# Optimization experiments

Measured on AMD Instinct MI355X. Metric: run time of the kernel, lower is better.

## Reference

```python
import jax, jax.numpy as jnp
import numpy as np

N, E = 50000, 800000          # nodes, directed edges (before self-loops)
IN, H, C = 128, 8, 32         # in_feats, heads, per-head channels (= h_feats)
G = 64                        # graphs in batch
NEG_SLOPE = 0.2               # PyG GATConv default leaky_relu slope


def setup_inputs() -> dict:
    key = jax.random.key(0)
    ks = jax.random.split(key, 8)
    x = jax.random.normal(ks[0], (N, IN), jnp.float32)
    edge_index = jax.random.randint(ks[1], (2, E), 0, N)
    batch = jnp.sort(jax.random.randint(ks[2], (N,), 0, G))
    W = jax.random.normal(ks[3], (IN, H * C), jnp.float32) * 0.05
    att_src = jax.random.normal(ks[4], (H, C), jnp.float32) * 0.1
    att_dst = jax.random.normal(ks[5], (H, C), jnp.float32) * 0.1
    bias = jnp.zeros((C,), jnp.float32)
    lin_w = jax.random.normal(ks[6], (C, 2), jnp.float32) * 0.1
    lin_b = jnp.zeros((2,), jnp.float32)
    return dict(x=x, edge_index=edge_index, batch=batch, W=W,
                att_src=att_src, att_dst=att_dst, bias=bias,
                lin_w=lin_w, lin_b=lin_b)


def gat_conv(x, edge_index, W, att_src, att_dst, bias):
    # PyG GATConv, heads=H, concat=False, add_self_loops=True
    n = x.shape[0]
    h = (x @ W).reshape(n, H, C)                      # [N,H,C]
    loops = jnp.arange(n, dtype=edge_index.dtype)
    src = jnp.concatenate([edge_index[0], loops])     # [E+N]
    dst = jnp.concatenate([edge_index[1], loops])
    a_src = jnp.einsum('nhc,hc->nh', h, att_src)      # [N,H]
    a_dst = jnp.einsum('nhc,hc->nh', h, att_dst)
    e = jax.nn.leaky_relu(a_src[src] + a_dst[dst], NEG_SLOPE)  # [E+N,H]
    # segment softmax over edges sharing the same destination node
    m = jax.ops.segment_max(e, dst, num_segments=n)
    m = jnp.where(jnp.isfinite(m), m, 0.0)            # guard isolated nodes
    w = jnp.exp(e - m[dst])
    denom = jax.ops.segment_sum(w, dst, num_segments=n)
    alpha = w / (denom[dst] + 1e-16)                  # [E+N,H]
    out = jax.ops.segment_sum(h[src] * alpha[:, :, None], dst, num_segments=n)  # [N,H,C]
    return out.mean(axis=1) + bias                    # concat=False -> head mean


def reference(x, edge_index, batch, W, att_src, att_dst, bias, lin_w, lin_b):
    hid = jax.nn.relu(gat_conv(x, edge_index, W, att_src, att_dst, bias))  # [N,C]
    sums = jax.ops.segment_sum(hid, batch, num_segments=G)                  # [G,C]
    cnt = jax.ops.segment_sum(jnp.ones((hid.shape[0],), hid.dtype), batch,
                              num_segments=G)
    pooled = sums / jnp.maximum(cnt, 1.0)[:, None]    # global_mean_pool
    # Dropout(0.5) is identity in eval mode
    x_t = pooled @ lin_w + lin_b                      # [G,2]
    return (x_t, pooled)
```

## Files before the change

kernel.cpp:

```cpp
#include <hip/hip_runtime.h>
#include <hip/hip_bf16.h>

#define N_NODES 50000
#define E_EDGES 800000
#define IN_F 128
#define H_HEADS 8
#define C_CH 32
#define HC 256
#define G_GRAPHS 64
#define NEG_SLOPE 0.2f

__global__ __launch_bounds__(256) void k_gemm(const float* __restrict__ x,
        const float* __restrict__ W, const float* __restrict__ att_src,
        const float* __restrict__ att_dst, float* __restrict__ h,
        float* __restrict__ a_src, float* __restrict__ a_dst) {
    __shared__ float xs[8 * IN_F];
    const int n0 = blockIdx.x * 8;
    const int tid = threadIdx.x;
    ((float4*)xs)[tid] = ((const float4*)(x + (size_t)n0 * IN_F))[tid];
    __syncthreads();

    const int j = tid;
    float acc[8];
    #pragma unroll
    for (int r = 0; r < 8; ++r) acc[r] = 0.f;

    const float4* xs4 = (const float4*)xs;
    for (int k4 = 0; k4 < IN_F / 4; ++k4) {
        const float w0 = W[(k4 * 4 + 0) * HC + j];
        const float w1 = W[(k4 * 4 + 1) * HC + j];
        const float w2 = W[(k4 * 4 + 2) * HC + j];
        const float w3 = W[(k4 * 4 + 3) * HC + j];
        #pragma unroll
        for (int r = 0; r < 8; ++r) {
            float4 xv = xs4[r * (IN_F / 4) + k4];
            acc[r] += xv.x * w0 + xv.y * w1 + xv.z * w2 + xv.w * w3;
        }
    }

    const float asv = att_src[j], adv = att_dst[j];
    const int hh = j >> 5;
    #pragma unroll
    for (int r = 0; r < 8; ++r) {
        h[(size_t)(n0 + r) * HC + j] = acc[r];
        float s = acc[r] * asv, d = acc[r] * adv;
        #pragma unroll
        for (int off = 16; off; off >>= 1) {
            s += __shfl_xor(s, off, 64);
            d += __shfl_xor(d, off, 64);
        }
        if ((tid & 31) == 0) {
            a_src[(n0 + r) * H_HEADS + hh] = s;
            a_dst[(n0 + r) * H_HEADS + hh] = d;
        }
    }
}

__global__ __launch_bounds__(256) void k_hist(const int* __restrict__ ei,
        int* __restrict__ deg) {
    int i = blockIdx.x * 256 + threadIdx.x;
    if (i < E_EDGES) atomicAdd(deg + ei[E_EDGES + i], 1);
}

__global__ __launch_bounds__(1024) void k_scan(const int* __restrict__ deg,
        int* __restrict__ off, int* __restrict__ cursor) {
    __shared__ int carry;
    __shared__ int wsum[16];
    const int tid = threadIdx.x, lane = tid & 63, wid = tid >> 6;
    if (tid == 0) carry = 0;
    __syncthreads();
    for (int base = 0; base < N_NODES; base += 1024) {
        int i = base + tid;
        int v = (i < N_NODES) ? deg[i] : 0;
        int s = v;
        #pragma unroll
        for (int d = 1; d < 64; d <<= 1) {
            int t = __shfl_up(s, d, 64);
            if (lane >= d) s += t;
        }
        if (lane == 63) wsum[wid] = s;
        __syncthreads();
        if (wid == 0 && lane < 16) {
            int t = wsum[lane];
            #pragma unroll
            for (int d = 1; d < 16; d <<= 1) {
                int u = __shfl_up(t, d, 64);
                if (lane >= d) t += u;
            }
            wsum[lane] = t;
        }
        __syncthreads();
        int wpre = wid ? wsum[wid - 1] : 0;
        int excl = carry + wpre + s - v;
        if (i < N_NODES) { off[i] = excl; cursor[i] = excl; }
        __syncthreads();
        if (tid == 0) carry += wsum[15];
        __syncthreads();
    }
    if (tid == 0) off[N_NODES] = E_EDGES;
}

__global__ __launch_bounds__(256) void k_scatter(const int* __restrict__ ei,
        int* __restrict__ cursor, int* __restrict__ csr_src) {
    int i = blockIdx.x * 256 + threadIdx.x;
    if (i >= E_EDGES) return;
    int dst = ei[E_EDGES + i];
    int p = atomicAdd(cursor + dst, 1);
    csr_src[p] = ei[i];
}

__global__ __launch_bounds__(256) void k_node(const float* __restrict__ h,
        const float* __restrict__ a_src, const float* __restrict__ a_dst,
        const int* __restrict__ off, const int* __restrict__ csr_src,
        const int* __restrict__ batch, const float* __restrict__ bias,
        float* __restrict__ pool, float* __restrict__ cnt) {
    const int wave = threadIdx.x >> 6, lane = threadIdx.x & 63;
    const int n = blockIdx.x * 4 + wave;
    if (n >= N_NODES) return;
    const int hh = lane >> 3;
    const int beg = off[n], end = off[n + 1];
    const float adst = a_dst[n * H_HEADS + hh];
    float es = a_src[n * H_HEADS + hh] + adst;
    const float e_self = es > 0.f ? es : NEG_SLOPE * es;

    float m = e_self;
    for (int k = beg; k < end; ++k) {
        int src = csr_src[k];
        float e = a_src[src * H_HEADS + hh] + adst;
        e = e > 0.f ? e : NEG_SLOPE * e;
        m = fmaxf(m, e);
    }

    float denom = 0.f;
    float4 acc = {0.f, 0.f, 0.f, 0.f};
    {
        float w = __expf(e_self - m);
        denom += w;
        float4 hv = ((const float4*)(h + (size_t)n * HC))[lane];
        acc.x += w * hv.x; acc.y += w * hv.y;
        acc.z += w * hv.z; acc.w += w * hv.w;
    }
    int k = beg;
    for (; k + 1 < end; k += 2) {
        int s0 = csr_src[k], s1 = csr_src[k + 1];
        float e0 = a_src[s0 * H_HEADS + hh] + adst;
        float e1 = a_src[s1 * H_HEADS + hh] + adst;
        e0 = e0 > 0.f ? e0 : NEG_SLOPE * e0;
        e1 = e1 > 0.f ? e1 : NEG_SLOPE * e1;
        float w0 = __expf(e0 - m);
        float w1 = __expf(e1 - m);
        float4 h0 = ((const float4*)(h + (size_t)s0 * HC))[lane];
        float4 h1 = ((const float4*)(h + (size_t)s1 * HC))[lane];
        denom += w0 + w1;
        acc.x += w0 * h0.x + w1 * h1.x;
        acc.y += w0 * h0.y + w1 * h1.y;
        acc.z += w0 * h0.z + w1 * h1.z;
        acc.w += w0 * h0.w + w1 * h1.w;
    }
    if (k < end) {
        int s0 = csr_src[k];
        float e0 = a_src[s0 * H_HEADS + hh] + adst;
        e0 = e0 > 0.f ? e0 : NEG_SLOPE * e0;
        float w0 = __expf(e0 - m);
        float4 h0 = ((const float4*)(h + (size_t)s0 * HC))[lane];
        denom += w0;
        acc.x += w0 * h0.x; acc.y += w0 * h0.y;
        acc.z += w0 * h0.z; acc.w += w0 * h0.w;
    }

    const float inv = 1.f / (denom + 1e-16f);
    float4 r = {acc.x * inv, acc.y * inv, acc.z * inv, acc.w * inv};
    #pragma unroll
    for (int o = 8; o < 64; o <<= 1) {
        r.x += __shfl_xor(r.x, o, 64);
        r.y += __shfl_xor(r.y, o, 64);
        r.z += __shfl_xor(r.z, o, 64);
        r.w += __shfl_xor(r.w, o, 64);
    }
    if (lane < 8) {
        const int c0 = lane * 4;
        const int g = batch[n];
        float o0 = fmaxf(r.x * 0.125f + bias[c0 + 0], 0.f);
        float o1 = fmaxf(r.y * 0.125f + bias[c0 + 1], 0.f);
        float o2 = fmaxf(r.z * 0.125f + bias[c0 + 2], 0.f);
        float o3 = fmaxf(r.w * 0.125f + bias[c0 + 3], 0.f);
        float* pg = pool + g * C_CH + c0;
        atomicAdd(pg + 0, o0); atomicAdd(pg + 1, o1);
        atomicAdd(pg + 2, o2); atomicAdd(pg + 3, o3);
        if (lane == 0) atomicAdd(cnt + g, 1.f);
    }
}

__global__ __launch_bounds__(256) void k_final(const float* __restrict__ pool,
        const float* __restrict__ cnt, const float* __restrict__ lin_w,
        const float* __restrict__ lin_b, float* __restrict__ out) {
    __shared__ float pd[G_GRAPHS * C_CH];
    int t = threadIdx.x;
    for (int i = t; i < G_GRAPHS * C_CH; i += 256) {
        int g = i >> 5;
        float p = pool[i] / fmaxf(cnt[g], 1.f);
        pd[i] = p;
        out[G_GRAPHS * 2 + i] = p;
    }
    __syncthreads();
    if (t < G_GRAPHS * 2) {
        int g = t >> 1, o = t & 1;
        float s = lin_b[o];
        #pragma unroll
        for (int c = 0; c < C_CH; ++c) s += pd[g * C_CH + c] * lin_w[c * 2 + o];
        out[t] = s;
    }
}

extern "C" void kernel_launch(void* const* d_in, const int* in_sizes, int n_in,
                              void* d_out, int out_size, void* d_ws, size_t ws_size,
                              hipStream_t stream) {
    const float* x       = (const float*)d_in[0];
    const int*   ei      = (const int*)d_in[1];
    const int*   batch   = (const int*)d_in[2];
    const float* W       = (const float*)d_in[3];
    const float* att_src = (const float*)d_in[4];
    const float* att_dst = (const float*)d_in[5];
    const float* bias    = (const float*)d_in[6];
    const float* lin_w   = (const float*)d_in[7];
    const float* lin_b   = (const float*)d_in[8];

    char* ws = (char*)d_ws;
    float* h       = (float*)(ws);
    float* a_src   = (float*)(ws + 51200000);
    float* a_dst   = (float*)(ws + 52800000);
    int*   deg     = (int*)  (ws + 54400000);
    int*   off     = (int*)  (ws + 54600000);
    int*   cursor  = (int*)  (ws + 54800064);
    int*   csr_src = (int*)  (ws + 55000064);
    float* pool    = (float*)(ws + 58200064);
    float* cnt     = (float*)(ws + 58208256);

    hipMemsetAsync(deg, 0, 200000, stream);
    hipMemsetAsync(pool, 0, 8192 + 256, stream);

    k_gemm<<<N_NODES / 8, 256, 0, stream>>>(x, W, att_src, att_dst, h, a_src, a_dst);
    k_hist<<<(E_EDGES + 255) / 256, 256, 0, stream>>>(ei, deg);
    k_scan<<<1, 1024, 0, stream>>>(deg, off, cursor);
    k_scatter<<<(E_EDGES + 255) / 256, 256, 0, stream>>>(ei, cursor, csr_src);
    k_node<<<(N_NODES + 3) / 4, 256, 0, stream>>>(
        h, a_src, a_dst, off, csr_src, batch, bias, pool, cnt);
    k_final<<<1, 256, 0, stream>>>(pool, cnt, lin_w, lin_b, (float*)d_out);
}
```

Measured before the change: 817.7 us.

## Store projected features as bf16, parallelize CSR scan, unroll edge gathers

The projected node features h are now stored as bf16 with round-to-nearest-even, which halves the bytes written by the GEMM and gathered per edge in the aggregation kernel. The single-block serial prefix scan is replaced by a per-chunk histogram, a tiny chunk scan and a 49-block local scan. The max and aggregation loops are unrolled by four so several gathers are in flight at once. Storing h in bf16 adds rounding error to the aggregated features, and the extra atomics on 49 chunk counters may contend.

```diff
diff --git a/kernel.cpp b/kernel.cpp
--- a/kernel.cpp
+++ b/kernel.cpp
@@ -9,10 +9,17 @@
 #define HC 256
 #define G_GRAPHS 64
 #define NEG_SLOPE 0.2f
+#define NCHUNK 49
+
+__device__ __forceinline__ unsigned short f2bf(float f) {
+    unsigned u = __float_as_uint(f);
+    u += 0x7fffu + ((u >> 16) & 1u);
+    return (unsigned short)(u >> 16);
+}
 
 __global__ __launch_bounds__(256) void k_gemm(const float* __restrict__ x,
         const float* __restrict__ W, const float* __restrict__ att_src,
-        const float* __restrict__ att_dst, float* __restrict__ h,
+        const float* __restrict__ att_dst, unsigned short* __restrict__ hb,
         float* __restrict__ a_src, float* __restrict__ a_dst) {
     __shared__ float xs[8 * IN_F];
     const int n0 = blockIdx.x * 8;
@@ -42,7 +49,7 @@
     const int hh = j >> 5;
     #pragma unroll
     for (int r = 0; r < 8; ++r) {
-        h[(size_t)(n0 + r) * HC + j] = acc[r];
+        hb[(size_t)(n0 + r) * HC + j] = f2bf(acc[r]);
         float s = acc[r] * asv, d = acc[r] * adv;
         #pragma unroll
         for (int off = 16; off; off >>= 1) {
@@ -57,47 +64,59 @@
 }
 
 __global__ __launch_bounds__(256) void k_hist(const int* __restrict__ ei,
-        int* __restrict__ deg) {
+        int* __restrict__ deg, int* __restrict__ chunk) {
     int i = blockIdx.x * 256 + threadIdx.x;
-    if (i < E_EDGES) atomicAdd(deg + ei[E_EDGES + i], 1);
-}
-
-__global__ __launch_bounds__(1024) void k_scan(const int* __restrict__ deg,
-        int* __restrict__ off, int* __restrict__ cursor) {
-    __shared__ int carry;
+    if (i >= E_EDGES) return;
+    int dst = ei[E_EDGES + i];
+    atomicAdd(deg + dst, 1);
+    atomicAdd(chunk + (dst >> 10), 1);
+}
+
+__global__ __launch_bounds__(64) void k_chunkscan(const int* __restrict__ chunk,
+        int* __restrict__ chunkoff) {
+    int t = threadIdx.x;
+    int v = (t < NCHUNK) ? chunk[t] : 0;
+    int s = v;
+    #pragma unroll
+    for (int d = 1; d < 64; d <<= 1) {
+        int u = __shfl_up(s, d, 64);
+        if (t >= d) s += u;
+    }
+    if (t < NCHUNK) chunkoff[t] = s - v;
+}
+
+__global__ __launch_bounds__(1024) void k_localscan(const int* __restrict__ deg,
+        const int* __restrict__ chunkoff, int* __restrict__ off,
+        int* __restrict__ cursor) {
     __shared__ int wsum[16];
     const int tid = threadIdx.x, lane = tid & 63, wid = tid >> 6;
-    if (tid == 0) carry = 0;
-    __syncthreads();
-    for (int base = 0; base < N_NODES; base += 1024) {
-        int i = base + tid;
-        int v = (i < N_NODES) ? deg[i] : 0;
-        int s = v;
-        #pragma unroll
-        for (int d = 1; d < 64; d <<= 1) {
-            int t = __shfl_up(s, d, 64);
-            if (lane >= d) s += t;
-        }
-        if (lane == 63) wsum[wid] = s;
-        __syncthreads();
-        if (wid == 0 && lane < 16) {
-            int t = wsum[lane];
-            #pragma unroll
-            for (int d = 1; d < 16; d <<= 1) {
-                int u = __shfl_up(t, d, 64);
-                if (lane >= d) t += u;
-            }
-            wsum[lane] = t;
-        }
-        __syncthreads();
-        int wpre = wid ? wsum[wid - 1] : 0;
-        int excl = carry + wpre + s - v;
-        if (i < N_NODES) { off[i] = excl; cursor[i] = excl; }
-        __syncthreads();
-        if (tid == 0) carry += wsum[15];
-        __syncthreads();
-    }
-    if (tid == 0) off[N_NODES] = E_EDGES;
+    const int i = blockIdx.x * 1024 + tid;
+    int v = (i < N_NODES) ? deg[i] : 0;
+    int s = v;
+    #pragma unroll
+    for (int d = 1; d < 64; d <<= 1) {
+        int t = __shfl_up(s, d, 64);
+        if (lane >= d) s += t;
+    }
+    if (lane == 63) wsum[wid] = s;
+    __syncthreads();
+    if (wid == 0 && lane < 16) {
+        int t = wsum[lane];
+        #pragma unroll
+        for (int d = 1; d < 16; d <<= 1) {
+            int u = __shfl_up(t, d, 64);
+            if (lane >= d) t += u;
+        }
+        wsum[lane] = t;
+    }
+    __syncthreads();
+    int wpre = wid ? wsum[wid - 1] : 0;
+    if (i < N_NODES) {
+        int excl = chunkoff[blockIdx.x] + wpre + s - v;
+        off[i] = excl;
+        cursor[i] = excl;
+    }
+    if (blockIdx.x == NCHUNK - 1 && tid == 0) off[N_NODES] = E_EDGES;
 }
 
 __global__ __launch_bounds__(256) void k_scatter(const int* __restrict__ ei,
@@ -109,7 +128,15 @@
     csr_src[p] = ei[i];
 }
 
-__global__ __launch_bounds__(256) void k_node(const float* __restrict__ h,
+__device__ __forceinline__ void bf4_unpack(uint2 q, float& x0, float& x1,
+                                           float& x2, float& x3) {
+    x0 = __uint_as_float(q.x << 16);
+    x1 = __uint_as_float(q.x & 0xffff0000u);
+    x2 = __uint_as_float(q.y << 16);
+    x3 = __uint_as_float(q.y & 0xffff0000u);
+}
+
+__global__ __launch_bounds__(256) void k_node(const unsigned short* __restrict__ hb,
         const float* __restrict__ a_src, const float* __restrict__ a_dst,
         const int* __restrict__ off, const int* __restrict__ csr_src,
         const int* __restrict__ batch, const float* __restrict__ bias,
@@ -124,7 +151,21 @@
     const float e_self = es > 0.f ? es : NEG_SLOPE * es;
 
     float m = e_self;
-    for (int k = beg; k < end; ++k) {
+    int k = beg;
+    for (; k + 3 < end; k += 4) {
+        int s0 = csr_src[k], s1 = csr_src[k + 1];
+        int s2 = csr_src[k + 2], s3 = csr_src[k + 3];
+        float e0 = a_src[s0 * H_HEADS + hh] + adst;
+        float e1 = a_src[s1 * H_HEADS + hh] + adst;
+        float e2 = a_src[s2 * H_HEADS + hh] + adst;
+        float e3 = a_src[s3 * H_HEADS + hh] + adst;
+        e0 = e0 > 0.f ? e0 : NEG_SLOPE * e0;
+        e1 = e1 > 0.f ? e1 : NEG_SLOPE * e1;
+        e2 = e2 > 0.f ? e2 : NEG_SLOPE * e2;
+        e3 = e3 > 0.f ? e3 : NEG_SLOPE * e3;
+        m = fmaxf(m, fmaxf(fmaxf(e0, e1), fmaxf(e2, e3)));
+    }
+    for (; k < end; ++k) {
         int src = csr_src[k];
         float e = a_src[src * H_HEADS + hh] + adst;
         e = e > 0.f ? e : NEG_SLOPE * e;
@@ -132,58 +173,60 @@
     }
 
     float denom = 0.f;
-    float4 acc = {0.f, 0.f, 0.f, 0.f};
+    float ax = 0.f, ay = 0.f, az = 0.f, aw = 0.f;
     {
         float w = __expf(e_self - m);
         denom += w;
-        float4 hv = ((const float4*)(h + (size_t)n * HC))[lane];
-        acc.x += w * hv.x; acc.y += w * hv.y;
-        acc.z += w * hv.z; acc.w += w * hv.w;
-    }
-    int k = beg;
-    for (; k + 1 < end; k += 2) {
-        int s0 = csr_src[k], s1 = csr_src[k + 1];
-        float e0 = a_src[s0 * H_HEADS + hh] + adst;
-        float e1 = a_src[s1 * H_HEADS + hh] + adst;
-        e0 = e0 > 0.f ? e0 : NEG_SLOPE * e0;
-        e1 = e1 > 0.f ? e1 : NEG_SLOPE * e1;
-        float w0 = __expf(e0 - m);
-        float w1 = __expf(e1 - m);
-        float4 h0 = ((const float4*)(h + (size_t)s0 * HC))[lane];
-        float4 h1 = ((const float4*)(h + (size_t)s1 * HC))[lane];
-        denom += w0 + w1;
-        acc.x += w0 * h0.x + w1 * h1.x;
-        acc.y += w0 * h0.y + w1 * h1.y;
-        acc.z += w0 * h0.z + w1 * h1.z;
-        acc.w += w0 * h0.w + w1 * h1.w;
-    }
-    if (k < end) {
-        int s0 = csr_src[k];
-        float e0 = a_src[s0 * H_HEADS + hh] + adst;
-        e0 = e0 > 0.f ? e0 : NEG_SLOPE * e0;
-        float w0 = __expf(e0 - m);
-        float4 h0 = ((const float4*)(h + (size_t)s0 * HC))[lane];
-        denom += w0;
-        acc.x += w0 * h0.x; acc.y += w0 * h0.y;
-        acc.z += w0 * h0.z; acc.w += w0 * h0.w;
+        uint2 q = ((const uint2*)(hb + (size_t)n * HC))[lane];
+        float x0, x1, x2, x3; bf4_unpack(q, x0, x1, x2, x3);
+        ax += w * x0; ay += w * x1; az += w * x2; aw += w * x3;
+    }
+    k = beg;
+    for (; k + 3 < end; k += 4) {
+        int s[4];
+        s[0] = csr_src[k]; s[1] = csr_src[k + 1];
+        s[2] = csr_src[k + 2]; s[3] = csr_src[k + 3];
+        uint2 q[4];
+        #pragma unroll
+        for (int u = 0; u < 4; ++u)
+            q[u] = ((const uint2*)(hb + (size_t)s[u] * HC))[lane];
+        #pragma unroll
+        for (int u = 0; u < 4; ++u) {
+            float e = a_src[s[u] * H_HEADS + hh] + adst;
+            e = e > 0.f ? e : NEG_SLOPE * e;
+            float w = __expf(e - m);
+            denom += w;
+            float x0, x1, x2, x3; bf4_unpack(q[u], x0, x1, x2, x3);
+            ax += w * x0; ay += w * x1; az += w * x2; aw += w * x3;
+        }
+    }
+    for (; k < end; ++k) {
+        int src = csr_src[k];
+        float e = a_src[src * H_HEADS + hh] + adst;
+        e = e > 0.f ? e : NEG_SLOPE * e;
+        float w = __expf(e - m);
+        denom += w;
+        uint2 q = ((const uint2*)(hb + (size_t)src * HC))[lane];
+        float x0, x1, x2, x3; bf4_unpack(q, x0, x1, x2, x3);
+        ax += w * x0; ay += w * x1; az += w * x2; aw += w * x3;
     }
 
     const float inv = 1.f / (denom + 1e-16f);
-    float4 r = {acc.x * inv, acc.y * inv, acc.z * inv, acc.w * inv};
+    float rx = ax * inv, ry = ay * inv, rz = az * inv, rw = aw * inv;
     #pragma unroll
     for (int o = 8; o < 64; o <<= 1) {
-        r.x += __shfl_xor(r.x, o, 64);
-        r.y += __shfl_xor(r.y, o, 64);
-        r.z += __shfl_xor(r.z, o, 64);
-        r.w += __shfl_xor(r.w, o, 64);
+        rx += __shfl_xor(rx, o, 64);
+        ry += __shfl_xor(ry, o, 64);
+        rz += __shfl_xor(rz, o, 64);
+        rw += __shfl_xor(rw, o, 64);
     }
     if (lane < 8) {
         const int c0 = lane * 4;
         const int g = batch[n];
-        float o0 = fmaxf(r.x * 0.125f + bias[c0 + 0], 0.f);
-        float o1 = fmaxf(r.y * 0.125f + bias[c0 + 1], 0.f);
-        float o2 = fmaxf(r.z * 0.125f + bias[c0 + 2], 0.f);
-        float o3 = fmaxf(r.w * 0.125f + bias[c0 + 3], 0.f);
+        float o0 = fmaxf(rx * 0.125f + bias[c0 + 0], 0.f);
+        float o1 = fmaxf(ry * 0.125f + bias[c0 + 1], 0.f);
+        float o2 = fmaxf(rz * 0.125f + bias[c0 + 2], 0.f);
+        float o3 = fmaxf(rw * 0.125f + bias[c0 + 3], 0.f);
         float* pg = pool + g * C_CH + c0;
         atomicAdd(pg + 0, o0); atomicAdd(pg + 1, o1);
         atomicAdd(pg + 2, o2); atomicAdd(pg + 3, o3);
@@ -226,24 +269,27 @@
     const float* lin_b   = (const float*)d_in[8];
 
     char* ws = (char*)d_ws;
-    float* h       = (float*)(ws);
-    float* a_src   = (float*)(ws + 51200000);
-    float* a_dst   = (float*)(ws + 52800000);
-    int*   deg     = (int*)  (ws + 54400000);
-    int*   off     = (int*)  (ws + 54600000);
-    int*   cursor  = (int*)  (ws + 54800064);
-    int*   csr_src = (int*)  (ws + 55000064);
-    float* pool    = (float*)(ws + 58200064);
-    float* cnt     = (float*)(ws + 58208256);
-
-    hipMemsetAsync(deg, 0, 200000, stream);
+    unsigned short* hb   = (unsigned short*)(ws);
+    float* a_src   = (float*)(ws + 25600000);
+    float* a_dst   = (float*)(ws + 27200000);
+    int*   deg     = (int*)  (ws + 28800000);
+    int*   chunk   = (int*)  (ws + 29000000);
+    int*   off     = (int*)  (ws + 29000256);
+    int*   cursor  = (int*)  (ws + 29200512);
+    int*   csr_src = (int*)  (ws + 29400512);
+    float* pool    = (float*)(ws + 32600512);
+    float* cnt     = (float*)(ws + 32608704);
+    int*   chunkoff= (int*)  (ws + 32608960);
+
+    hipMemsetAsync(deg, 0, 200256, stream);
     hipMemsetAsync(pool, 0, 8192 + 256, stream);
 
-    k_gemm<<<N_NODES / 8, 256, 0, stream>>>(x, W, att_src, att_dst, h, a_src, a_dst);
-    k_hist<<<(E_EDGES + 255) / 256, 256, 0, stream>>>(ei, deg);
-    k_scan<<<1, 1024, 0, stream>>>(deg, off, cursor);
+    k_gemm<<<N_NODES / 8, 256, 0, stream>>>(x, W, att_src, att_dst, hb, a_src, a_dst);
+    k_hist<<<(E_EDGES + 255) / 256, 256, 0, stream>>>(ei, deg, chunk);
+    k_chunkscan<<<1, 64, 0, stream>>>(chunk, chunkoff);
+    k_localscan<<<NCHUNK, 1024, 0, stream>>>(deg, chunkoff, off, cursor);
     k_scatter<<<(E_EDGES + 255) / 256, 256, 0, stream>>>(ei, cursor, csr_src);
     k_node<<<(N_NODES + 3) / 4, 256, 0, stream>>>(
-        h, a_src, a_dst, off, csr_src, batch, bias, pool, cnt);
+        hb, a_src, a_dst, off, csr_src, batch, bias, pool, cnt);
     k_final<<<1, 256, 0, stream>>>(pool, cnt, lin_w, lin_b, (float*)d_out);
 }
```

After: 1.808 ms. 121% more time.
